# Optimization experiments

Hardware: AMD Instinct MI355X
Metric: run time of the kernel (lower is better)

Reference implementation:

```python
import jax, jax.numpy as jnp
import numpy as np

P_THRESHOLD = 0.6
K_CAP = 16


def softmax_m1(x):
    # f(x) = (exp(x)-1) / sum(exp(x)-1), as in the torch module
    fx = jnp.expm1(x)
    return fx / fx.sum(-1, keepdims=True)


def align_chars(start_map, nb_map, max_ch):
    # eval-mode recurrence of NeighborDecoder.align_chars, run for a fixed
    # max_ch steps (no data-dependent early break; char_masks carry the
    # finished state exactly as in torch).
    b = start_map.shape[0]

    def step(carry, i):
        char_map, finished = carry  # [b, N+1], [b] int32
        mask = (finished == 0).astype(char_map.dtype)
        out = (char_map, mask)  # emitted BEFORE the update, matching torch
        finished = finished + (char_map[:, -1] > P_THRESHOLD).astype(jnp.int32)
        kk = jnp.minimum(1 + 2 * i, K_CAP).astype(char_map.dtype)
        cmd = softmax_m1(jax.lax.stop_gradient(char_map) * kk)  # .detach() in torch
        nxt = jnp.einsum('bn,bnm->bm', cmd, nb_map)
        return (nxt, finished), out

    init = (start_map, jnp.zeros(b, jnp.int32))
    _, (maps, masks) = jax.lax.scan(step, init, jnp.arange(max_ch))
    return maps.transpose(1, 0, 2), masks.T  # [b, T, N+1], [b, T]


def setup_inputs() -> dict:
    key = jax.random.key(0)
    ks = jax.random.split(key, 8)
    b, c, h, w = 32, 384, 16, 64
    num_classes = 97
    s = 1.0 / np.sqrt(c)
    return {
        'x': jax.random.normal(ks[0], (b, c, h, w), jnp.float32),
        'eos_emb': (jax.random.normal(ks[1], (c,), jnp.float32) * 0.02),
        'q_w': jax.random.normal(ks[2], (c, c), jnp.float32) * s,
        'q_b': jnp.zeros((c,), jnp.float32),
        'k_w': jax.random.normal(ks[3], (c, c), jnp.float32) * s,
        'k_b': jnp.zeros((c,), jnp.float32),
        'nav_w': jax.random.normal(ks[4], (1, c, c), jnp.float32) * 0.01,
        'nav_b': jnp.zeros((1,), jnp.float32),
        'cls_w': jax.random.normal(ks[5], (num_classes, c), jnp.float32) * s,
        'cls_b': jnp.zeros((num_classes,), jnp.float32),
        'max_char': 48,
    }


def reference(x, eos_emb, q_w, q_b, k_w, k_b, nav_w, nav_b, cls_w, cls_b, max_char):
    b, c, h, w = x.shape
    scale = float(c) ** 0.5
    xt = x.reshape(b, c, h * w).transpose(0, 2, 1)  # [b, N, c]
    g = xt.mean(axis=1)  # [b, c]
    x_ext = jnp.concatenate(
        [xt, jnp.broadcast_to(eos_emb, (b, 1, c))], axis=1)  # [b, N+1, c]

    q_start = g @ q_w.T + q_b                      # [b, c]
    k_feat = x_ext @ k_w.T + k_b                   # [b, N+1, c]
    start_map = jnp.einsum('bnc,bc->bn', k_feat, q_start) / scale
    start_map = jax.nn.softmax(start_map, axis=1)  # [b, N+1]

    q_feat = xt @ q_w.T + q_b                      # [b, N, c]
    # BilinearLayer with out=1: einsum('bim,mn,bjn->bij') + bias
    nb_map = jnp.einsum('bim,mn,bjn->bij', q_feat, nav_w[0], k_feat) + nav_b[0]
    nb_map = jax.nn.softmax(nb_map / scale, axis=2)  # [b, N, N+1]

    last = jnp.zeros((h * w + 1,), x.dtype).at[-1].set(1.0)
    nb_map = jnp.concatenate(
        [nb_map, jnp.broadcast_to(last, (b, 1, h * w + 1))], axis=1)  # [b, N+1, N+1]

    char_maps, char_masks = align_chars(start_map, nb_map, max_char)
    char_feats = jnp.einsum('btn,bnc->btc', char_maps, x_ext)
    char_feats = char_feats * char_masks[..., None]
    logits = char_feats @ cls_w.T + cls_b          # [b, T, num_classes]
    return logits, char_feats, char_maps, char_masks, nb_map
```

## Files before the change

### kernel.cpp

```cpp
#include <hip/hip_runtime.h>
#include <cstdint>
#include <cstddef>

#define BB   32
#define CC   384
#define NN   1024
#define N1   1025
#define TT   48
#define NCLS 97
#define NBL_LD 1088
#define NBTS   1056

static constexpr float INV_SCALE = 1.0f / 19.595917942265423f;

using bf16x8 = __attribute__((ext_vector_type(8))) __bf16;
using f32x4  = __attribute__((ext_vector_type(4))) float;

static constexpr size_t OFF_LOGITS = 0;
static constexpr size_t OFF_CFEAT  = 148992;
static constexpr size_t OFF_CMAPS  = 738816;
static constexpr size_t OFF_CMASK  = 2313216;
static constexpr size_t OFF_NB     = 2314752;

static constexpr size_t OFF_XB     = 0;
static constexpr size_t OFF_WGEM   = 25165824;
static constexpr size_t OFF_BIAS   = 25755648;
static constexpr size_t OFF_G      = 25758720;
static constexpr size_t OFF_QSTART = 25807872;
static constexpr size_t OFF_KEOS   = 25857024;
static constexpr size_t OFF_STATS  = 25858560;
static constexpr size_t OFF_MAPSBF = 26120704;
static constexpr size_t OFF_CMD    = 29266432;
static constexpr size_t OFF_PSUM   = 29536768;
static constexpr size_t OFF_XBT    = 29569536;
static constexpr size_t OFF_NBL    = 29569536;
static constexpr size_t OFF_OUT    = 100942336;
static constexpr size_t OFF_NBT    = 100942336;

__device__ __forceinline__ float bf2f(uint u) {
    union { uint i; float f; } v; v.i = u << 16; return v.f;
}
__device__ __forceinline__ ushort f2bf(float f) {
    union { float f; uint i; } v; v.f = f;
    uint r = v.i + 0x7fffu + ((v.i >> 16) & 1u);
    return (ushort)(r >> 16);
}

__global__ __launch_bounds__(256) void k_conv_mean(
    const float* __restrict__ x, ushort* __restrict__ xb, float* __restrict__ g)
{
    int row  = blockIdx.x * 4 + (threadIdx.x >> 6);
    int lane = threadIdx.x & 63;
    const float* src = x + (size_t)row * NN;
    ushort* dst = xb + (size_t)row * NN;
    float s = 0.f;
#pragma unroll
    for (int q = 0; q < 4; q++) {
        float4 v = ((const float4*)src)[q * 64 + lane];
        s += v.x + v.y + v.z + v.w;
        ushort4 p; p.x = f2bf(v.x); p.y = f2bf(v.y); p.z = f2bf(v.z); p.w = f2bf(v.w);
        ((ushort4*)dst)[q * 64 + lane] = p;
    }
#pragma unroll
    for (int o = 32; o; o >>= 1) s += __shfl_down(s, o);
    if (lane == 0) g[row] = s * (1.0f / NN);
}

__global__ __launch_bounds__(256) void k_transpose(
    const ushort* __restrict__ xb, ushort* __restrict__ xbT)
{
    int b = blockIdx.z, c0 = blockIdx.x * 64, n0 = blockIdx.y * 64;
    __shared__ ushort t[64][65];
    int ur = threadIdx.x >> 5, uc = threadIdx.x & 31;
    const ushort* src = xb + ((size_t)b * CC + c0) * NN + n0;
#pragma unroll
    for (int p = 0; p < 8; p++) {
        int c = p * 8 + ur;
        uint v = ((const uint*)(src + (size_t)c * NN))[uc];
        t[c][uc * 2]     = (ushort)(v & 0xffffu);
        t[c][uc * 2 + 1] = (ushort)(v >> 16);
    }
    __syncthreads();
    ushort* dst = xbT + ((size_t)b * N1 + n0) * CC + c0;
#pragma unroll
    for (int p = 0; p < 8; p++) {
        int n = p * 8 + ur;
        uint v = (uint)t[uc * 2][n] | (((uint)t[uc * 2 + 1][n]) << 16);
        ((uint*)(dst + (size_t)n * CC))[uc] = v;
    }
}

__global__ void k_eosrow(const float* __restrict__ eos, ushort* __restrict__ xbT)
{
    int c = threadIdx.x;
    xbT[((size_t)blockIdx.x * N1 + NN) * CC + c] = f2bf(eos[c]);
}

__global__ void k_wk(const float* __restrict__ k_w, const float* __restrict__ k_b,
                     ushort* __restrict__ Wgem, float* __restrict__ bias)
{
    int j = blockIdx.x, c = threadIdx.x;
    Wgem[(size_t)j * CC + c] = f2bf(k_w[(size_t)j * CC + c]);
    if (c == 0) bias[j] = k_b[j];
}

__global__ void k_w2(const float* __restrict__ nav_w, const float* __restrict__ q_w,
                     const float* __restrict__ q_b, ushort* __restrict__ Wgem,
                     float* __restrict__ bias)
{
    int m = blockIdx.x, c = threadIdx.x;
    float acc = 0.f, accb = 0.f;
    for (int k = 0; k < CC; k++) {
        float nv = nav_w[(size_t)k * CC + m];
        acc  += nv * q_w[(size_t)k * CC + c];
        accb += nv * q_b[k];
    }
    Wgem[(size_t)(CC + m) * CC + c] = f2bf(acc);
    if (c == 0) bias[CC + m] = accb;
}

__global__ void k_qstart(const float* __restrict__ g, const float* __restrict__ q_w,
                         const float* __restrict__ q_b, float* __restrict__ q_start)
{
    int b = blockIdx.x, k = threadIdx.x;
    __shared__ float gs[CC];
    gs[k] = g[(size_t)b * CC + k];
    __syncthreads();
    float acc = q_b[k];
    const float* w = q_w + (size_t)k * CC;
    for (int c = 0; c < CC; c++) acc += gs[c] * w[c];
    q_start[(size_t)b * CC + k] = acc;
}

__global__ void k_keos(const float* __restrict__ eos, const float* __restrict__ k_w,
                       const float* __restrict__ k_b, float* __restrict__ keos,
                       ushort* __restrict__ Out)
{
    int co = threadIdx.x;
    float acc = k_b[co];
    const float* w = k_w + (size_t)co * CC;
    for (int c = 0; c < CC; c++) acc += eos[c] * w[c];
    keos[co] = acc;
    ushort v = f2bf(acc);
    for (int b = 0; b < BB; b++) Out[((size_t)b * N1 + NN) * 768 + co] = v;
}

template<int MODE, int NTN, int PERB>
__global__ __launch_bounds__(256) void k_gemm(
    const ushort* __restrict__ Aall, size_t strideAb, int lda,
    const ushort* __restrict__ Ball, size_t strideBb, int ldb,
    ushort* __restrict__ Cout, size_t strideCb, int ldc,
    const float* __restrict__ bias)
{
    int wid = blockIdx.x;
    int xcd = wid & 7;
    int work = xcd * (PERB * 4) + (wid >> 3);
    int b = work / PERB;
    int r = work - b * PERB;
    int m0 = (r / NTN) * 128, n0 = (r % NTN) * 128;

    const ushort* A  = Aall + (size_t)b * strideAb;
    const ushort* Bp = Ball + (size_t)b * strideBb;
    __shared__ ushort sbuf[16384];
    ushort* As = sbuf;
    ushort* Bs = sbuf + 8192;
    int tid = threadIdx.x, wave = tid >> 6, lane = tid & 63;
    int wm = wave >> 1, wn = wave & 1;
    f32x4 acc[4][4] = {};

    uint4 ra[4], rb[4];
    auto load_tiles = [&](int k0) {
#pragma unroll
        for (int q = 0; q < 4; q++) {
            int idx = q * 256 + tid, rr = idx >> 3, c8 = (idx & 7) * 8;
            ra[q] = *(const uint4*)(A  + (size_t)(m0 + rr) * lda + k0 + c8);
            rb[q] = *(const uint4*)(Bp + (size_t)(n0 + rr) * ldb + k0 + c8);
        }
    };
    load_tiles(0);
    for (int k0 = 0; k0 < CC; k0 += 64) {
        __syncthreads();
#pragma unroll
        for (int q = 0; q < 4; q++) {
            int idx = q * 256 + tid, rr = idx >> 3, ch = idx & 7;
            int sw = (ch ^ (rr & 7)) << 3;
            *(uint4*)(As + rr * 64 + sw) = ra[q];
            *(uint4*)(Bs + rr * 64 + sw) = rb[q];
        }
        __syncthreads();
        if (k0 + 64 < CC) load_tiles(k0 + 64);
#pragma unroll
        for (int h = 0; h < 2; h++) {
            bf16x8 af[4], bfr[4];
            int chb = h * 4 + (lane >> 4);
#pragma unroll
            for (int i = 0; i < 4; i++) {
                int row = wm * 64 + i * 16 + (lane & 15);
                af[i]  = *(const bf16x8*)(As + row * 64 + ((chb ^ (row & 7)) << 3));
                int col = wn * 64 + i * 16 + (lane & 15);
                bfr[i] = *(const bf16x8*)(Bs + col * 64 + ((chb ^ (col & 7)) << 3));
            }
#pragma unroll
            for (int i = 0; i < 4; i++)
#pragma unroll
                for (int j = 0; j < 4; j++)
                    acc[i][j] = __builtin_amdgcn_mfma_f32_16x16x32_bf16(af[i], bfr[j], acc[i][j], 0, 0, 0);
        }
    }
    __syncthreads();
#pragma unroll
    for (int i = 0; i < 4; i++) {
        int rl = wm * 64 + i * 16 + ((lane >> 4) << 2);
#pragma unroll
        for (int j = 0; j < 4; j++) {
            int cl = wn * 64 + j * 16 + (lane & 15);
            float bv = (MODE == 0) ? bias[n0 + cl] : 0.f;
#pragma unroll
            for (int rr = 0; rr < 4; rr++) {
                float val = (MODE == 0) ? (acc[i][j][rr] + bv) : (acc[i][j][rr] * INV_SCALE);
                sbuf[(rl + rr) * 128 + cl] = f2bf(val);
            }
        }
    }
    __syncthreads();
    ushort* Cb = Cout + (size_t)b * strideCb;
#pragma unroll
    for (int q = 0; q < 8; q++) {
        int idx = q * 256 + tid, row = idx >> 4, seg = idx & 15;
        *(uint4*)(Cb + (size_t)(m0 + row) * ldc + n0 + seg * 8) =
            *(const uint4*)(sbuf + row * 128 + seg * 8);
    }
}

__global__ __launch_bounds__(1024) void k_start(
    const ushort* __restrict__ Out, const float* __restrict__ q_start,
    float* __restrict__ cmaps)
{
    int b = blockIdx.x, tid = threadIdx.x;
    __shared__ float qs[CC];
    __shared__ float red[16];
    __shared__ float bc;
    if (tid < CC) qs[tid] = q_start[(size_t)b * CC + tid];
    __syncthreads();
    auto dot = [&](int n) {
        const uint4* row = (const uint4*)(Out + ((size_t)b * N1 + n) * 768);
        float acc = 0.f;
        for (int c8 = 0; c8 < CC / 8; c8++) {
            uint4 u = row[c8];
            const ushort* us = (const ushort*)&u;
#pragma unroll
            for (int e = 0; e < 8; e++) acc += bf2f(us[e]) * qs[c8 * 8 + e];
        }
        return acc * INV_SCALE;
    };
    float v0 = dot(tid);
    float v1 = (tid == 0) ? dot(1024) : -1e30f;
    float lm = fmaxf(v0, v1);
#pragma unroll
    for (int o = 32; o; o >>= 1) lm = fmaxf(lm, __shfl_down(lm, o));
    if ((tid & 63) == 0) red[tid >> 6] = lm;
    __syncthreads();
    if (tid == 0) { float m = red[0]; for (int i = 1; i < 16; i++) m = fmaxf(m, red[i]); bc = m; }
    __syncthreads();
    float bmax = bc;
    float e0 = __expf(v0 - bmax);
    float e1 = (tid == 0) ? __expf(v1 - bmax) : 0.f;
    float ls = e0 + e1;
#pragma unroll
    for (int o = 32; o; o >>= 1) ls += __shfl_down(ls, o);
    if ((tid & 63) == 0) red[tid >> 6] = ls;
    __syncthreads();
    if (tid == 0) { float s = 0.f; for (int i = 0; i < 16; i++) s += red[i]; bc = s; }
    __syncthreads();
    float inv = 1.f / bc;
    float* o = cmaps + ((size_t)b * TT) * N1;
    o[tid] = e0 * inv;
    if (tid == 0) o[1024] = e1 * inv;
}

__global__ __launch_bounds__(256) void k_eoscol_nbl(
    const ushort* __restrict__ Out, const float* __restrict__ keos, ushort* __restrict__ nbL)
{
    int gw = blockIdx.x * 4 + (threadIdx.x >> 6);
    int lane = threadIdx.x & 63;
    for (int rr = 0; rr < 4; rr++) {
        int gi = gw * 4 + rr, b = gi >> 10, i = gi & 1023;
        const ushort* row = Out + ((size_t)b * N1 + i) * 768 + 384;
        float acc = 0.f;
        for (int c = lane; c < CC; c += 64) acc += bf2f(row[c]) * keos[c];
#pragma unroll
        for (int o = 32; o; o >>= 1) acc += __shfl_down(acc, o);
        if (lane == 0) nbL[((size_t)b * N1 + i) * NBL_LD + 1024] = f2bf(acc * INV_SCALE);
    }
}

__global__ __launch_bounds__(256) void k_softnb2(
    const ushort* __restrict__ nbL, float* __restrict__ nb, float2* __restrict__ stats)
{
    int bi = blockIdx.x;
    int b = bi >> 10, i = bi & 1023;
    const ushort* row = nbL + ((size_t)b * N1 + i) * NBL_LD;
    int tid = threadIdx.x;
    uint2 u = *(const uint2*)(row + tid * 4);
    float v0 = bf2f(u.x & 0xffffu), v1 = bf2f(u.x >> 16);
    float v2 = bf2f(u.y & 0xffffu), v3 = bf2f(u.y >> 16);
    float vt = (tid == 0) ? bf2f(row[1024]) : -1e30f;
    __shared__ float r1[4]; __shared__ float bc;
    float lm = fmaxf(fmaxf(fmaxf(v0, v1), fmaxf(v2, v3)), vt);
#pragma unroll
    for (int o = 32; o; o >>= 1) lm = fmaxf(lm, __shfl_down(lm, o));
    if ((tid & 63) == 0) r1[tid >> 6] = lm;
    __syncthreads();
    if (tid == 0) bc = fmaxf(fmaxf(r1[0], r1[1]), fmaxf(r1[2], r1[3]));
    __syncthreads();
    float m = bc;
    float e0 = __expf(v0 - m), e1 = __expf(v1 - m), e2 = __expf(v2 - m), e3 = __expf(v3 - m);
    float et = (tid == 0) ? __expf(vt - m) : 0.f;
    float s = e0 + e1 + e2 + e3 + et;
#pragma unroll
    for (int o = 32; o; o >>= 1) s += __shfl_down(s, o);
    if ((tid & 63) == 0) r1[tid >> 6] = s;
    __syncthreads();
    if (tid == 0) bc = r1[0] + r1[1] + r1[2] + r1[3];
    __syncthreads();
    float inv = 1.f / bc;
    float* orow = nb + ((size_t)b * N1 + i) * N1;
    float4 ov = make_float4(e0 * inv, e1 * inv, e2 * inv, e3 * inv);
    *(float4*)(orow + tid * 4) = ov;
    if (tid == 0) { orow[1024] = et * inv; stats[b * 1024 + i] = make_float2(m, inv); }
}

__global__ void k_onehot(float* __restrict__ nb)
{
    int b = blockIdx.x;
    float* row = nb + ((size_t)b * N1 + NN) * N1;
    for (int j = threadIdx.x; j < N1; j += 256)
        row[j] = (j == 1024) ? 1.f : 0.f;
}

__global__ __launch_bounds__(256) void k_transq(
    const ushort* __restrict__ nbL, const float2* __restrict__ stats,
    ushort* __restrict__ nbT)
{
    int b = blockIdx.z, n0 = blockIdx.x * 64, j0 = blockIdx.y * 64;
    __shared__ ushort tile[64][80];
    __shared__ float2 st[64];
    int tid = threadIdx.x;
    if (tid < 64) st[tid] = stats[b * 1024 + n0 + tid];
    __syncthreads();
#pragma unroll
    for (int q = 0; q < 2; q++) {
        int idx = q * 256 + tid, rl = idx >> 3, ch = idx & 7;
        const ushort* src = nbL + ((size_t)b * N1 + n0 + rl) * NBL_LD + j0 + ch * 8;
        uint4 u = *(const uint4*)src;
        float2 s = st[rl];
        const ushort* us = (const ushort*)&u;
#pragma unroll
        for (int k = 0; k < 8; k++)
            tile[ch * 8 + k][rl] = f2bf(__expf(bf2f(us[k]) - s.x) * s.y);
    }
    __syncthreads();
#pragma unroll
    for (int q = 0; q < 2; q++) {
        int idx = q * 256 + tid, jl = idx >> 3, seg = idx & 7;
        int j = j0 + jl;
        if (j <= 1024) {
            uint4 v = *(const uint4*)&tile[jl][seg * 8];
            *(uint4*)(nbT + ((size_t)b * N1 + j) * NBTS + n0 + seg * 8) = v;
        }
    }
}

__global__ __launch_bounds__(256) void k_cmd0(
    const float* __restrict__ cmaps, float* __restrict__ cmd_out, float* __restrict__ ps_out)
{
    int b = blockIdx.x, tid = threadIdx.x;
    __shared__ float red[4];
    const float* m = cmaps + (size_t)b * TT * N1;
    float s = 0.f;
    for (int n = tid; n < N1; n += 256) {
        float c = expm1f(m[n]);
        cmd_out[(size_t)b * 1056 + n] = c;
        s += c;
    }
#pragma unroll
    for (int o = 32; o; o >>= 1) s += __shfl_down(s, o);
    if ((tid & 63) == 0) red[tid >> 6] = s;
    __syncthreads();
    if (tid == 0) ps_out[b * 128] = red[0] + red[1] + red[2] + red[3];
    else if (tid < 128) ps_out[b * 128 + tid] = 0.f;
}

__device__ __forceinline__ float dot16(uint4 r0, uint4 r1,
                                       const float* cA, const float* cB)
{
    const ushort* p0 = (const ushort*)&r0;
    const ushort* p1 = (const ushort*)&r1;
    float acc = 0.f;
#pragma unroll
    for (int e = 0; e < 8; e++) acc += bf2f(p0[e]) * cA[e];
#pragma unroll
    for (int e = 0; e < 8; e++) acc += bf2f(p1[e]) * cB[e];
    return acc;
}

__global__ __launch_bounds__(256) void k_step4(
    float* __restrict__ cmaps, const ushort* __restrict__ nbT,
    const float* __restrict__ cmd_in, float* __restrict__ cmd_out,
    const float* __restrict__ ps_in, float* __restrict__ ps_out, int t)
{
    int b = blockIdx.y, blk = blockIdx.x;
    int tid = threadIdx.x, wave = tid >> 6, lane = tid & 63;
    int j0 = blk * 32 + wave * 8;
    const ushort* base = nbT + (size_t)b * N1 * NBTS;

    uint4 rv[8][2];
#pragma unroll
    for (int r = 0; r < 8; ++r) {
        int j = j0 + r; if (j > 1024) j = 1024;
        const ushort* row = base + (size_t)j * NBTS;
        rv[r][0] = *(const uint4*)(row + lane * 8);
        rv[r][1] = *(const uint4*)(row + 512 + lane * 8);
    }
    const float* ci = cmd_in + (size_t)b * 1056;
    float cA[8], cB[8];
    *(float4*)&cA[0] = *(const float4*)(ci + lane * 8);
    *(float4*)&cA[4] = *(const float4*)(ci + lane * 8 + 4);
    *(float4*)&cB[0] = *(const float4*)(ci + 512 + lane * 8);
    *(float4*)&cB[4] = *(const float4*)(ci + 512 + lane * 8 + 4);
    float ctail = ci[1024];

    __shared__ float sred;
    __shared__ float red[4];
    if (wave == 0) {
        float pv = (lane < 33) ? ps_in[b * 128 + lane] : 0.f;
#pragma unroll
        for (int o = 32; o; o >>= 1) pv += __shfl_down(pv, o);
        if (lane == 0) sred = pv;
    }

    float acc[8];
#pragma unroll
    for (int r = 0; r < 8; ++r) {
        float a = dot16(rv[r][0], rv[r][1], cA, cB);
#pragma unroll
        for (int o = 32; o; o >>= 1) a += __shfl_down(a, o);
        acc[r] = a;
    }
    __syncthreads();
    float inv = 1.f / sred;
    int kkn = 3 + 2 * t; if (kkn > 16) kkn = 16;
    if (lane == 0) {
        float cs = 0.f;
        float* orow = cmaps + ((size_t)b * TT + t + 1) * N1;
        float* co = cmd_out + (size_t)b * 1056;
#pragma unroll
        for (int r = 0; r < 8; ++r) {
            int j = j0 + r;
            if (j <= 1024) {
                float s = acc[r] + ((j == 1024) ? ctail : 0.f);
                float mo = s * inv;
                orow[j] = mo;
                float cn = expm1f((float)kkn * mo);
                co[j] = cn;
                cs += cn;
            }
        }
        red[wave] = cs;
    }
    __syncthreads();
    if (tid == 0)
        ps_out[b * 128 + blk] = red[0] + red[1] + red[2] + red[3];
}

__global__ void k_masks(const float* __restrict__ cmaps, float* __restrict__ cmask)
{
    int b = threadIdx.x;
    if (b < BB) {
        int fin = 0;
        for (int t = 0; t < TT; t++) {
            cmask[b * TT + t] = (fin == 0) ? 1.f : 0.f;
            fin += (cmaps[((size_t)b * TT + t) * N1 + 1024] > 0.6f) ? 1 : 0;
        }
    }
}

__global__ void k_mapsbf(const float* __restrict__ cmaps, ushort* __restrict__ mb)
{
    size_t i = (size_t)blockIdx.x * 256 + threadIdx.x;
    size_t bt = i >> 10; int n = (int)(i & 1023);
    mb[i] = f2bf(cmaps[bt * N1 + n]);
}

__global__ __launch_bounds__(256) void k_cfeat(
    const ushort* __restrict__ mapsbf, const ushort* __restrict__ xb,
    const float* __restrict__ cmaps, const float* __restrict__ eos,
    const float* __restrict__ masks, float* __restrict__ cfeat)
{
    int b = blockIdx.x;
    int wave = threadIdx.x >> 6, lane = threadIdx.x & 63;
    f32x4 acc[3][6] = {};
    const ushort* Ab = mapsbf + (size_t)b * TT * 1024;
    const ushort* Bb = xb + (size_t)b * CC * NN;
    for (int k0 = 0; k0 < NN; k0 += 32) {
        int kk_ = k0 + (lane >> 4) * 8;
        bf16x8 af[3], bfr[6];
#pragma unroll
    for (int i = 0; i < 3; i++)
            af[i] = *(const bf16x8*)(Ab + (size_t)(i * 16 + (lane & 15)) * 1024 + kk_);
#pragma unroll
        for (int j = 0; j < 6; j++)
            bfr[j] = *(const bf16x8*)(Bb + (size_t)(wave * 96 + j * 16 + (lane & 15)) * NN + kk_);
#pragma unroll
        for (int i = 0; i < 3; i++)
#pragma unroll
            for (int j = 0; j < 6; j++)
                acc[i][j] = __builtin_amdgcn_mfma_f32_16x16x32_bf16(af[i], bfr[j], acc[i][j], 0, 0, 0);
    }
#pragma unroll
    for (int i = 0; i < 3; i++) {
        int tbase = i * 16 + ((lane >> 4) << 2);
#pragma unroll
        for (int j = 0; j < 6; j++) {
            int c = wave * 96 + j * 16 + (lane & 15);
            float ev = eos[c];
#pragma unroll
            for (int rr = 0; rr < 4; rr++) {
                int tt = tbase + rr;
                float mlast = cmaps[((size_t)b * TT + tt) * N1 + 1024];
                float val = (acc[i][j][rr] + mlast * ev) * masks[b * TT + tt];
                cfeat[((size_t)b * TT + tt) * CC + c] = val;
            }
        }
    }
}

__global__ __launch_bounds__(128) void k_logits(
    const float* __restrict__ cfeat, const float* __restrict__ cls_w,
    const float* __restrict__ cls_b, float* __restrict__ out)
{
    int bt = blockIdx.x;
    __shared__ float row[CC];
    for (int c = threadIdx.x; c < CC; c += 128) row[c] = cfeat[(size_t)bt * CC + c];
    __syncthreads();
    int j = threadIdx.x;
    if (j < NCLS) {
        float acc = cls_b[j];
        const float* w = cls_w + (size_t)j * CC;
        for (int c = 0; c < CC; c++) acc += row[c] * w[c];
        out[(size_t)bt * NCLS + j] = acc;
    }
}

extern "C" void kernel_launch(void* const* d_in, const int* in_sizes, int n_in,
                              void* d_out, int out_size, void* d_ws, size_t ws_size,
                              hipStream_t stream)
{
    (void)in_sizes; (void)n_in; (void)out_size; (void)ws_size;
    const float* x     = (const float*)d_in[0];
    const float* eos   = (const float*)d_in[1];
    const float* q_w   = (const float*)d_in[2];
    const float* q_b   = (const float*)d_in[3];
    const float* k_w   = (const float*)d_in[4];
    const float* k_b   = (const float*)d_in[5];
    const float* nav_w = (const float*)d_in[6];
    const float* cls_w = (const float*)d_in[8];
    const float* cls_b = (const float*)d_in[9];

    char* ws = (char*)d_ws;
    ushort* xb     = (ushort*)(ws + OFF_XB);
    ushort* Wgem   = (ushort*)(ws + OFF_WGEM);
    float*  bias   = (float*)(ws + OFF_BIAS);
    float*  g      = (float*)(ws + OFF_G);
    float*  qstart = (float*)(ws + OFF_QSTART);
    float*  keos   = (float*)(ws + OFF_KEOS);
    float2* stats  = (float2*)(ws + OFF_STATS);
    ushort* mapsbf = (ushort*)(ws + OFF_MAPSBF);
    float*  cmdbuf = (float*)(ws + OFF_CMD);
    float*  psbuf  = (float*)(ws + OFF_PSUM);
    ushort* xbT    = (ushort*)(ws + OFF_XBT);
    ushort* nbL    = (ushort*)(ws + OFF_NBL);
    ushort* Out    = (ushort*)(ws + OFF_OUT);
    ushort* nbT    = (ushort*)(ws + OFF_NBT);

    float* out     = (float*)d_out;
    float* logits  = out + OFF_LOGITS;
    float* cfeat   = out + OFF_CFEAT;
    float* cmaps   = out + OFF_CMAPS;
    float* cmask   = out + OFF_CMASK;
    float* nb      = out + OFF_NB;

    k_conv_mean<<<3072, 256, 0, stream>>>(x, xb, g);
    k_transpose<<<dim3(6, 16, BB), 256, 0, stream>>>(xb, xbT);
    k_eosrow<<<BB, CC, 0, stream>>>(eos, xbT);
    k_wk<<<CC, CC, 0, stream>>>(k_w, k_b, Wgem, bias);
    k_w2<<<CC, CC, 0, stream>>>(nav_w, q_w, q_b, Wgem, bias);
    k_qstart<<<BB, CC, 0, stream>>>(g, q_w, q_b, qstart);
    k_keos<<<1, CC, 0, stream>>>(eos, k_w, k_b, keos, Out);

    k_gemm<0, 6, 48><<<1536, 256, 0, stream>>>(
        xbT, (size_t)N1 * CC, CC, Wgem, 0, CC, Out, (size_t)N1 * 768, 768, bias);

    k_start<<<BB, 1024, 0, stream>>>(Out, qstart, cmaps);
    k_cmd0<<<BB, 256, 0, stream>>>(cmaps, cmdbuf, psbuf);
    k_eoscol_nbl<<<2048, 256, 0, stream>>>(Out, keos, nbL);

    k_gemm<1, 8, 64><<<2048, 256, 0, stream>>>(
        Out + 384, (size_t)N1 * 768, 768, Out, (size_t)N1 * 768, 768,
        nbL, (size_t)N1 * NBL_LD, NBL_LD, nullptr);

    k_softnb2<<<BB * NN, 256, 0, stream>>>(nbL, nb, stats);
    k_onehot<<<BB, 256, 0, stream>>>(nb);
    k_transq<<<dim3(16, 17, BB), 256, 0, stream>>>(nbL, stats, nbT);

    for (int t = 0; t < TT - 1; t++)
        k_step4<<<dim3(33, BB), 256, 0, stream>>>(
            cmaps, nbT,
            cmdbuf + (size_t)(t & 1) * 33792, cmdbuf + (size_t)((t + 1) & 1) * 33792,
            psbuf + (size_t)(t & 1) * 4096,  psbuf + (size_t)((t + 1) & 1) * 4096, t);

    k_masks<<<1, 64, 0, stream>>>(cmaps, cmask);
    k_mapsbf<<<6144, 256, 0, stream>>>(cmaps, mapsbf);
    k_cfeat<<<BB, 256, 0, stream>>>(mapsbf, xb, cmaps, eos, cmask, cfeat);
    k_logits<<<BB * TT, 128, 0, stream>>>(cfeat, cls_w, cls_b, logits);
}
```

Measured before the change: 1.202 ms.

## Merge setup kernels into one launch and use direct global-to-LDS loads in GEMM

Folds five small setup kernels (weight conversion, nav/q weight product, eos row, key-eos projection, q_start) into one branch-dispatched kernel, removing four launches. The GEMM tile loads now go straight from global memory into LDS via global_load_lds, with the XOR swizzle moved to the source address, instead of staging through registers. The old register-prefetch overlap of the next tile is gone, so each k-step now waits on its own load.

```diff
diff --git a/kernel.cpp b/kernel.cpp
--- a/kernel.cpp
+++ b/kernel.cpp
@@ -46,6 +46,12 @@
     return (ushort)(r >> 16);
 }
 
+__device__ __forceinline__ void gld16(const ushort* g, ushort* l) {
+    __builtin_amdgcn_global_load_lds(
+        (const __attribute__((address_space(1))) uint*)g,
+        (__attribute__((address_space(3))) uint*)l, 16, 0, 0);
+}
+
 __global__ __launch_bounds__(256) void k_conv_mean(
     const float* __restrict__ x, ushort* __restrict__ xb, float* __restrict__ g)
 {
@@ -90,59 +96,49 @@
     }
 }
 
-__global__ void k_eosrow(const float* __restrict__ eos, ushort* __restrict__ xbT)
-{
-    int c = threadIdx.x;
-    xbT[((size_t)blockIdx.x * N1 + NN) * CC + c] = f2bf(eos[c]);
-}
-
-__global__ void k_wk(const float* __restrict__ k_w, const float* __restrict__ k_b,
-                     ushort* __restrict__ Wgem, float* __restrict__ bias)
-{
-    int j = blockIdx.x, c = threadIdx.x;
-    Wgem[(size_t)j * CC + c] = f2bf(k_w[(size_t)j * CC + c]);
-    if (c == 0) bias[j] = k_b[j];
-}
-
-__global__ void k_w2(const float* __restrict__ nav_w, const float* __restrict__ q_w,
-                     const float* __restrict__ q_b, ushort* __restrict__ Wgem,
-                     float* __restrict__ bias)
-{
-    int m = blockIdx.x, c = threadIdx.x;
-    float acc = 0.f, accb = 0.f;
-    for (int k = 0; k < CC; k++) {
-        float nv = nav_w[(size_t)k * CC + m];
-        acc  += nv * q_w[(size_t)k * CC + c];
-        accb += nv * q_b[k];
-    }
-    Wgem[(size_t)(CC + m) * CC + c] = f2bf(acc);
-    if (c == 0) bias[CC + m] = accb;
-}
-
-__global__ void k_qstart(const float* __restrict__ g, const float* __restrict__ q_w,
-                         const float* __restrict__ q_b, float* __restrict__ q_start)
-{
-    int b = blockIdx.x, k = threadIdx.x;
-    __shared__ float gs[CC];
-    gs[k] = g[(size_t)b * CC + k];
-    __syncthreads();
-    float acc = q_b[k];
-    const float* w = q_w + (size_t)k * CC;
-    for (int c = 0; c < CC; c++) acc += gs[c] * w[c];
-    q_start[(size_t)b * CC + k] = acc;
-}
-
-__global__ void k_keos(const float* __restrict__ eos, const float* __restrict__ k_w,
-                       const float* __restrict__ k_b, float* __restrict__ keos,
-                       ushort* __restrict__ Out)
-{
-    int co = threadIdx.x;
-    float acc = k_b[co];
-    const float* w = k_w + (size_t)co * CC;
-    for (int c = 0; c < CC; c++) acc += eos[c] * w[c];
-    keos[co] = acc;
-    ushort v = f2bf(acc);
-    for (int b = 0; b < BB; b++) Out[((size_t)b * N1 + NN) * 768 + co] = v;
+__global__ __launch_bounds__(384) void k_setup(
+    const float* __restrict__ k_w, const float* __restrict__ k_b,
+    const float* __restrict__ nav_w, const float* __restrict__ q_w,
+    const float* __restrict__ q_b, const float* __restrict__ eos,
+    const float* __restrict__ g,
+    ushort* __restrict__ Wgem, float* __restrict__ bias,
+    ushort* __restrict__ xbT, float* __restrict__ keos,
+    ushort* __restrict__ Out, float* __restrict__ q_start)
+{
+    int blk = blockIdx.x, c = threadIdx.x;
+    if (blk < 384) {
+        Wgem[(size_t)blk * CC + c] = f2bf(k_w[(size_t)blk * CC + c]);
+        if (c == 0) bias[blk] = k_b[blk];
+    } else if (blk < 768) {
+        int m = blk - 384;
+        float acc = 0.f, accb = 0.f;
+        for (int k = 0; k < CC; k++) {
+            float nv = nav_w[(size_t)k * CC + m];
+            acc  += nv * q_w[(size_t)k * CC + c];
+            accb += nv * q_b[k];
+        }
+        Wgem[(size_t)(CC + m) * CC + c] = f2bf(acc);
+        if (c == 0) bias[CC + m] = accb;
+    } else if (blk < 800) {
+        int b = blk - 768;
+        xbT[((size_t)b * N1 + NN) * CC + c] = f2bf(eos[c]);
+    } else if (blk == 800) {
+        float acc = k_b[c];
+        const float* w = k_w + (size_t)c * CC;
+        for (int k = 0; k < CC; k++) acc += eos[k] * w[k];
+        keos[c] = acc;
+        ushort v = f2bf(acc);
+        for (int b = 0; b < BB; b++) Out[((size_t)b * N1 + NN) * 768 + c] = v;
+    } else {
+        int b = blk - 801;
+        __shared__ float gs[CC];
+        gs[c] = g[(size_t)b * CC + c];
+        __syncthreads();
+        float acc = q_b[c];
+        const float* w = q_w + (size_t)c * CC;
+        for (int k = 0; k < CC; k++) acc += gs[k] * w[k];
+        q_start[(size_t)b * CC + c] = acc;
+    }
 }
 
 template<int MODE, int NTN, int PERB>
@@ -168,27 +164,17 @@
     int wm = wave >> 1, wn = wave & 1;
     f32x4 acc[4][4] = {};
 
-    uint4 ra[4], rb[4];
-    auto load_tiles = [&](int k0) {
+    for (int k0 = 0; k0 < CC; k0 += 64) {
 #pragma unroll
         for (int q = 0; q < 4; q++) {
-            int idx = q * 256 + tid, rr = idx >> 3, c8 = (idx & 7) * 8;
-            ra[q] = *(const uint4*)(A  + (size_t)(m0 + rr) * lda + k0 + c8);
-            rb[q] = *(const uint4*)(Bp + (size_t)(n0 + rr) * ldb + k0 + c8);
-        }
-    };
-    load_tiles(0);
-    for (int k0 = 0; k0 < CC; k0 += 64) {
+            int idx = q * 256 + tid, rr = idx >> 3, sw = idx & 7;
+            int src = (sw ^ (rr & 7)) << 3;
+            ushort* dA = As + (size_t)(q * 2048 + wave * 512);
+            ushort* dB = Bs + (size_t)(q * 2048 + wave * 512);
+            gld16(A  + (size_t)(m0 + rr) * lda + k0 + src, dA);
+            gld16(Bp + (size_t)(n0 + rr) * ldb + k0 + src, dB);
+        }
         __syncthreads();
-#pragma unroll
-        for (int q = 0; q < 4; q++) {
-            int idx = q * 256 + tid, rr = idx >> 3, ch = idx & 7;
-            int sw = (ch ^ (rr & 7)) << 3;
-            *(uint4*)(As + rr * 64 + sw) = ra[q];
-            *(uint4*)(Bs + rr * 64 + sw) = rb[q];
-        }
-        __syncthreads();
-        if (k0 + 64 < CC) load_tiles(k0 + 64);
 #pragma unroll
         for (int h = 0; h < 2; h++) {
             bf16x8 af[4], bfr[4];
@@ -206,8 +192,8 @@
                 for (int j = 0; j < 4; j++)
                     acc[i][j] = __builtin_amdgcn_mfma_f32_16x16x32_bf16(af[i], bfr[j], acc[i][j], 0, 0, 0);
         }
-    }
-    __syncthreads();
+        __syncthreads();
+    }
 #pragma unroll
     for (int i = 0; i < 4; i++) {
         int rl = wm * 64 + i * 16 + ((lane >> 4) << 2);
@@ -506,7 +492,7 @@
         int kk_ = k0 + (lane >> 4) * 8;
         bf16x8 af[3], bfr[6];
 #pragma unroll
-    for (int i = 0; i < 3; i++)
+        for (int i = 0; i < 3; i++)
             af[i] = *(const bf16x8*)(Ab + (size_t)(i * 16 + (lane & 15)) * 1024 + kk_);
 #pragma unroll
         for (int j = 0; j < 6; j++)
@@ -592,11 +578,8 @@
 
     k_conv_mean<<<3072, 256, 0, stream>>>(x, xb, g);
     k_transpose<<<dim3(6, 16, BB), 256, 0, stream>>>(xb, xbT);
-    k_eosrow<<<BB, CC, 0, stream>>>(eos, xbT);
-    k_wk<<<CC, CC, 0, stream>>>(k_w, k_b, Wgem, bias);
-    k_w2<<<CC, CC, 0, stream>>>(nav_w, q_w, q_b, Wgem, bias);
-    k_qstart<<<BB, CC, 0, stream>>>(g, q_w, q_b, qstart);
-    k_keos<<<1, CC, 0, stream>>>(eos, k_w, k_b, keos, Out);
+    k_setup<<<833, 384, 0, stream>>>(k_w, k_b, nav_w, q_w, q_b, eos, g,
+                                     Wgem, bias, xbT, keos, Out, qstart);
 
     k_gemm<0, 6, 48><<<1536, 256, 0, stream>>>(
         xbT, (size_t)N1 * CC, CC, Wgem, 0, CC, Out, (size_t)N1 * 768, 768, bias);
```

New measurement: 1.038 ms. 13.6% less time.
